# Kernel optimization log

Measured on AMD Instinct MI355X. Metric: run time of the kernel, lower is better.

## Reference

```python
import jax, jax.numpy as jnp
import numpy as np
from jax import nn as jnn

N = 100000      # nodes
E = 3200000     # edges (avg degree 32)
G = 1024        # graphs in batch
F_IN = 3        # num_features (hard-coded in module)
D = 32          # dim (hard-coded in module)
BN_EPS = 1e-5


def setup_inputs() -> dict:
    key = jax.random.key(0)
    ks = jax.random.split(key, 24)
    def lin(k, i, o):
        return (jax.random.normal(k, (i, o), jnp.float32) / np.sqrt(i)).astype(jnp.float32)
    inp = {}
    inp["x"] = jax.random.normal(ks[0], (N, F_IN), jnp.float32)
    inp["edge_index"] = jax.random.randint(ks[1], (2, E), 0, N, dtype=jnp.int32)
    inp["batch"] = jnp.sort(jax.random.randint(ks[2], (N,), 0, G, dtype=jnp.int32))
    idx = 3
    in_dims = [F_IN, D, D]
    for l in (1, 2, 3):
        inp[f"W{l}a"] = lin(ks[idx], in_dims[l - 1], D); idx += 1
        inp[f"b{l}a"] = jnp.zeros((D,), jnp.float32)
        inp[f"W{l}b"] = lin(ks[idx], D, D); idx += 1
        inp[f"b{l}b"] = jnp.zeros((D,), jnp.float32)
        inp[f"g{l}"] = jnp.ones((D,), jnp.float32)            # BN gamma
        inp[f"be{l}"] = jnp.zeros((D,), jnp.float32)          # BN beta
        inp[f"m{l}"] = 0.1 * jax.random.normal(ks[idx], (D,), jnp.float32); idx += 1  # running mean
        inp[f"v{l}"] = jax.random.uniform(ks[idx], (D,), jnp.float32, 0.5, 1.5); idx += 1  # running var
    inp["Wf1"] = lin(ks[idx], D, D); idx += 1
    inp["bf1"] = jnp.zeros((D,), jnp.float32)
    inp["Wf2"] = lin(ks[idx], D, 1)
    inp["bf2"] = jnp.zeros((1,), jnp.float32)
    return inp


def reference(x, edge_index, batch,
              W1a, b1a, W1b, b1b, g1, be1, m1, v1,
              W2a, b2a, W2b, b2b, g2, be2, m2, v2,
              W3a, b3a, W3b, b3b, g3, be3, m3, v3,
              Wf1, bf1, Wf2, bf2):
    src, dst = edge_index[0], edge_index[1]

    def gin_bn(h, Wa, ba, Wb, bb, g, be, m, v):
        # GINConv (eps=0): nn(x + sum_{j->i} x_j); then relu; then BatchNorm1d (eval stats)
        agg = jax.ops.segment_sum(h[src], dst, num_segments=N) + h  # [N, d]
        h2 = jnn.relu(agg @ Wa + ba) @ Wb + bb                      # 2-layer MLP
        h2 = jnn.relu(h2)
        return g * (h2 - m) * jax.lax.rsqrt(v + BN_EPS) + be

    h = gin_bn(x, W1a, b1a, W1b, b1b, g1, be1, m1, v1)
    h = gin_bn(h, W2a, b2a, W2b, b2b, g2, be2, m2, v2)
    h = gin_bn(h, W3a, b3a, W3b, b3b, g3, be3, m3, v3)
    p = jax.ops.segment_sum(h, batch, num_segments=G)   # global_add_pool -> [G, D]
    p = jnn.relu(p @ Wf1 + bf1)
    # dropout p=0.5 is identity at inference
    return jnp.tanh(p @ Wf2 + bf2)                      # [G, 1]
```

## Files before the change

### kernel.cpp

```cpp
#include <hip/hip_runtime.h>
#include <math.h>

#define D 32
#define BN_EPS 1e-5f
#define NRANGE 512
#define RWC 196
#define MAXD 80
#define EPB 8192
#define K1_TPB 512
#define EPT (EPB / K1_TPB)
#define PCH 8

__global__ __launch_bounds__(K1_TPB) void build_part(
    const int* __restrict__ src, const int* __restrict__ dst,
    unsigned int* __restrict__ part, int* __restrict__ gcount,
    int E, int cap, int RW, unsigned long long M) {
    __shared__ unsigned int sorted[EPB];
    __shared__ unsigned short rid[EPB];
    __shared__ int cnt[NRANGE];
    __shared__ int exc[NRANGE];
    __shared__ int cur[NRANGE];
    __shared__ int gbase[NRANGE];
    int t = threadIdx.x;
    cnt[t] = 0;
    __syncthreads();

    int base = blockIdx.x * EPB;
    int n = min(EPB, E - base);

    unsigned int mypk[EPT];
    unsigned short myr[EPT];
#pragma unroll
    for (int k = 0; k < EPT; k++) {
        int i = t + k * K1_TPB;
        if (i < n) {
            int d = dst[base + i];
            int s = src[base + i];
            int r = (int)(((unsigned long long)d * M) >> 40);
            mypk[k] = ((unsigned)(d - r * RW) << 17) | (unsigned)s;
            myr[k] = (unsigned short)r;
            atomicAdd(&cnt[r], 1);
        } else myr[k] = 0xFFFFu;
    }
    __syncthreads();

    int inc = cnt[t];
    exc[t] = inc;
    __syncthreads();
    for (int s = 1; s < NRANGE; s <<= 1) {
        int u = (t >= s) ? exc[t - s] : 0;
        __syncthreads();
        exc[t] += u;
        __syncthreads();
    }
    int excl = exc[t] - cnt[t];
    __syncthreads();
    exc[t] = excl;
    cur[t] = excl;
    gbase[t] = atomicAdd(&gcount[t], cnt[t]);
    __syncthreads();

#pragma unroll
    for (int k = 0; k < EPT; k++) {
        if (myr[k] != 0xFFFFu) {
            int j = atomicAdd(&cur[myr[k]], 1);
            sorted[j] = mypk[k];
            rid[j] = myr[k];
        }
    }
    __syncthreads();

    for (int j = t; j < n; j += K1_TPB) {
        int r = rid[j];
        int pos = gbase[r] + (j - exc[r]);
        if (pos < cap) part[(size_t)r * cap + pos] = sorted[j];
    }
}

__global__ __launch_bounds__(1024) void build_csr(
    const unsigned int* __restrict__ part, const int* __restrict__ gcount,
    int* __restrict__ col, int* __restrict__ deg,
    int cap, int RW, int N, int maxd) {
    __shared__ int bucket[RWC * MAXD];
    __shared__ int rank_[RWC];
    int r = blockIdx.x, t = threadIdx.x, T = blockDim.x;
    for (int i = t; i < RW; i += T) rank_[i] = 0;
    __syncthreads();

    int count = gcount[r]; if (count > cap) count = cap;
    const unsigned int* p = part + (size_t)r * cap;
    int nbase = r * RW;
    for (int i = t; i < count; i += T) {
        unsigned int v = p[i];
        int dl = (int)(v >> 17);
        int slot = atomicAdd(&rank_[dl], 1);
        if (slot < maxd) bucket[dl * maxd + slot] = (int)(v & 0x1FFFFu);
    }
    __syncthreads();

    for (int i = t; i < RW; i += T) {
        int rk = rank_[i]; if (rk > maxd) rk = maxd;
        int pdg = (rk + 15) & ~15; if (pdg > maxd) pdg = maxd;
        int self = nbase + i;
        for (int k = rk; k < pdg; k++) bucket[i * maxd + k] = self;
    }
    __syncthreads();

    int nvalid = N - nbase; if (nvalid > RW) nvalid = RW;
    if (nvalid <= 0) return;
    int words = nvalid * maxd;
    int4* dst4 = (int4*)&col[(size_t)nbase * maxd];
    const int4* src4 = (const int4*)bucket;
    int nq = words >> 2;
    for (int i = t; i < nq; i += T) dst4[i] = src4[i];
    for (int i = t; i < nvalid; i += T) {
        int rk = rank_[i];
        deg[nbase + i] = rk < maxd ? rk : maxd;
    }
}

__global__ void compute_y(const float* __restrict__ x, const float* __restrict__ W1a,
                          float* __restrict__ y, int N) {
    long long gid = (long long)blockIdx.x * blockDim.x + threadIdx.x;
    int i = (int)(gid >> 5);
    int lane = (int)(gid & 31);
    if (i >= N) return;
    float x0 = x[i * 3 + 0], x1 = x[i * 3 + 1], x2 = x[i * 3 + 2];
    float t = x0 * W1a[0 * D + lane];
    t = fmaf(x1, W1a[1 * D + lane], t);
    t = fmaf(x2, W1a[2 * D + lane], t);
    y[(size_t)i * D + lane] = t;
}

template <bool SKIP_WA>
__global__ void layer_fused(const float* __restrict__ hin, const int* __restrict__ deg,
                            const int* __restrict__ col, int maxd,
                            const float* __restrict__ Wa, const float* __restrict__ ba,
                            const float* __restrict__ Wb, const float* __restrict__ bb,
                            const float* __restrict__ g, const float* __restrict__ be,
                            const float* __restrict__ m, const float* __restrict__ v,
                            float* __restrict__ hout, int N) {
    long long gid = (long long)blockIdx.x * blockDim.x + threadIdx.x;
    int i = (int)(gid >> 5);
    int lane = (int)(gid & 31);
    if (i >= N) return;

    int dg = deg[i];
    if (dg > maxd) dg = maxd;
    int pdg = (dg + 15) & ~15; if (pdg > maxd) pdg = maxd;
    float acc = hin[(size_t)i * D + lane] * (float)(1 + dg - pdg);
    const int* cp = &col[(size_t)i * maxd];
    int e = 0;
    for (; e + 32 <= pdg; e += 32) {
        int4 c0 = *(const int4*)&cp[e];
        int4 c1 = *(const int4*)&cp[e + 4];
        int4 c2 = *(const int4*)&cp[e + 8];
        int4 c3 = *(const int4*)&cp[e + 12];
        int4 c4 = *(const int4*)&cp[e + 16];
        int4 c5 = *(const int4*)&cp[e + 20];
        int4 c6 = *(const int4*)&cp[e + 24];
        int4 c7 = *(const int4*)&cp[e + 28];
        float a0 = hin[(size_t)c0.x * D + lane];
        float a1 = hin[(size_t)c0.y * D + lane];
        float a2 = hin[(size_t)c0.z * D + lane];
        float a3 = hin[(size_t)c0.w * D + lane];
        float a4 = hin[(size_t)c1.x * D + lane];
        float a5 = hin[(size_t)c1.y * D + lane];
        float a6 = hin[(size_t)c1.z * D + lane];
        float a7 = hin[(size_t)c1.w * D + lane];
        float a8 = hin[(size_t)c2.x * D + lane];
        float a9 = hin[(size_t)c2.y * D + lane];
        float a10 = hin[(size_t)c2.z * D + lane];
        float a11 = hin[(size_t)c2.w * D + lane];
        float a12 = hin[(size_t)c3.x * D + lane];
        float a13 = hin[(size_t)c3.y * D + lane];
        float a14 = hin[(size_t)c3.z * D + lane];
        float a15 = hin[(size_t)c3.w * D + lane];
        float a16 = hin[(size_t)c4.x * D + lane];
        float a17 = hin[(size_t)c4.y * D + lane];
        float a18 = hin[(size_t)c4.z * D + lane];
        float a19 = hin[(size_t)c4.w * D + lane];
        float a20 = hin[(size_t)c5.x * D + lane];
        float a21 = hin[(size_t)c5.y * D + lane];
        float a22 = hin[(size_t)c5.z * D + lane];
        float a23 = hin[(size_t)c5.w * D + lane];
        float a24 = hin[(size_t)c6.x * D + lane];
        float a25 = hin[(size_t)c6.y * D + lane];
        float a26 = hin[(size_t)c6.z * D + lane];
        float a27 = hin[(size_t)c6.w * D + lane];
        float a28 = hin[(size_t)c7.x * D + lane];
        float a29 = hin[(size_t)c7.y * D + lane];
        float a30 = hin[(size_t)c7.z * D + lane];
        float a31 = hin[(size_t)c7.w * D + lane];
        acc += (((a0 + a1) + (a2 + a3)) + ((a4 + a5) + (a6 + a7))) +
               (((a8 + a9) + (a10 + a11)) + ((a12 + a13) + (a14 + a15))) +
               (((a16 + a17) + (a18 + a19)) + ((a20 + a21) + (a22 + a23))) +
               (((a24 + a25) + (a26 + a27)) + ((a28 + a29) + (a30 + a31)));
    }
    for (; e + 16 <= pdg; e += 16) {
        int4 c0 = *(const int4*)&cp[e];
        int4 c1 = *(const int4*)&cp[e + 4];
        int4 c2 = *(const int4*)&cp[e + 8];
        int4 c3 = *(const int4*)&cp[e + 12];
        float a0 = hin[(size_t)c0.x * D + lane];
        float a1 = hin[(size_t)c0.y * D + lane];
        float a2 = hin[(size_t)c0.z * D + lane];
        float a3 = hin[(size_t)c0.w * D + lane];
        float a4 = hin[(size_t)c1.x * D + lane];
        float a5 = hin[(size_t)c1.y * D + lane];
        float a6 = hin[(size_t)c1.z * D + lane];
        float a7 = hin[(size_t)c1.w * D + lane];
        float a8 = hin[(size_t)c2.x * D + lane];
        float a9 = hin[(size_t)c2.y * D + lane];
        float aa = hin[(size_t)c2.z * D + lane];
        float ab = hin[(size_t)c2.w * D + lane];
        float ac = hin[(size_t)c3.x * D + lane];
        float ad = hin[(size_t)c3.y * D + lane];
        float ae = hin[(size_t)c3.z * D + lane];
        float af = hin[(size_t)c3.w * D + lane];
        acc += ((a0 + a1) + (a2 + a3)) + ((a4 + a5) + (a6 + a7)) +
               (((a8 + a9) + (aa + ab)) + ((ac + ad) + (ae + af)));
    }

    float t;
    if (SKIP_WA) {
        t = fmaxf(acc + ba[lane], 0.f);
    } else {
        t = ba[lane];
#pragma unroll
        for (int k = 0; k < D; k++) {
            float ak = __shfl(acc, k, D);
            t = fmaf(ak, Wa[k * D + lane], t);
        }
        t = fmaxf(t, 0.f);
    }
    float o = bb[lane];
#pragma unroll
    for (int j = 0; j < D; j++) {
        float tj = __shfl(t, j, D);
        o = fmaf(tj, Wb[j * D + lane], o);
    }
    o = fmaxf(o, 0.f);
    hout[(size_t)i * D + lane] =
        g[lane] * (o - m[lane]) * rsqrtf(v[lane] + BN_EPS) + be[lane];
}

__device__ __forceinline__ int lower_bound_i(const int* a, int n, int key) {
    int lo = 0, hi = n;
    while (lo < hi) {
        int mid = (lo + hi) >> 1;
        if (a[mid] < key) lo = mid + 1; else hi = mid;
    }
    return lo;
}

__global__ void pool_partial(const float* __restrict__ h, const int* __restrict__ batch,
                             float* __restrict__ pool, int N, int G) {
    long long gid = (long long)blockIdx.x * blockDim.x + threadIdx.x;
    int grp = (int)(gid >> 5);
    int lane = (int)(gid & 31);
    int gi = grp / PCH;
    int c = grp - gi * PCH;
    if (gi >= G) return;
    int lo = lower_bound_i(batch, N, gi);
    int hi = lower_bound_i(batch, N, gi + 1);
    int len = hi - lo;
    if (len <= 0) return;
    int chunk = (len + PCH - 1) / PCH;
    int s = lo + c * chunk;
    int e = s + chunk; if (e > hi) e = hi;
    if (s >= e) return;
    float p = 0.f;
    for (int n = s; n < e; n++) p += h[(size_t)n * D + lane];
    atomicAdd(&pool[(size_t)gi * D + lane], p);
}

__global__ void head_kernel(const float* __restrict__ pool, const float* __restrict__ Wf1,
                            const float* __restrict__ bf1, const float* __restrict__ Wf2,
                            const float* __restrict__ bf2, float* __restrict__ out, int G) {
    long long gid = (long long)blockIdx.x * blockDim.x + threadIdx.x;
    int gi = (int)(gid >> 5);
    int lane = (int)(gid & 31);
    if (gi >= G) return;
    float p = pool[(size_t)gi * D + lane];
    float q = bf1[lane];
#pragma unroll
    for (int j = 0; j < D; j++) {
        float pj = __shfl(p, j, D);
        q = fmaf(pj, Wf1[j * D + lane], q);
    }
    q = fmaxf(q, 0.f);
    float r = q * Wf2[lane];
#pragma unroll
    for (int off = 16; off; off >>= 1) r += __shfl_xor(r, off, D);
    if (lane == 0) out[gi] = tanhf(r + bf2[0]);
}

extern "C" void kernel_launch(void* const* d_in, const int* in_sizes, int n_in,
                              void* d_out, int out_size, void* d_ws, size_t ws_size,
                              hipStream_t stream) {
    const float* x = (const float*)d_in[0];
    const int* ei = (const int*)d_in[1];
    const int* batch = (const int*)d_in[2];
    const int E = in_sizes[1] / 2;
    const int N = in_sizes[2];
    const int G = out_size;
    const int* src = ei;
    const int* dst = ei + E;

    const float* P[3][8];
    for (int l = 0; l < 3; l++)
        for (int k = 0; k < 8; k++) P[l][k] = (const float*)d_in[3 + 8 * l + k];
    const float* Wf1 = (const float*)d_in[27];
    const float* bf1 = (const float*)d_in[28];
    const float* Wf2 = (const float*)d_in[29];
    const float* bf2 = (const float*)d_in[30];

    const int RW = (N + NRANGE - 1) / NRANGE;
    const unsigned long long M = ((1ull << 40) + RW - 1) / RW;
    int mean = (E + NRANGE - 1) / NRANGE;
    int cap = mean + mean / 8 + 64;
    cap = (cap + 7) & ~7;

    float* ws = (float*)d_ws;
    size_t off = 0;
    float* h0 = ws + off; off += (size_t)N * D;
    float* h1 = ws + off; off += (size_t)N * D;
    unsigned int* part = (unsigned int*)h0;
    int* deg = (int*)(ws + off); off += N;
    int* gcount = (int*)(ws + off); off += NRANGE;
    float* pool = ws + off; off += (size_t)G * D;
    int* col = (int*)(ws + off);
    size_t remaining = ws_size / 4 > off ? ws_size / 4 - off : 0;
    int maxd = (int)(remaining / (size_t)N);
    if (maxd > MAXD) maxd = MAXD;
    maxd &= ~15;
    if (maxd < 16) maxd = 16;

    const int B = 256;
    long long tN32 = (long long)N * D;
    int nbp = (E + EPB - 1) / EPB;

    hipMemsetAsync(gcount, 0, NRANGE * sizeof(int), stream);
    build_part<<<nbp, K1_TPB, 0, stream>>>(src, dst, part, gcount, E, cap, RW, M);
    build_csr<<<NRANGE, 1024, 0, stream>>>(part, gcount, col, deg, cap, RW, N, maxd);

    compute_y<<<(int)((tN32 + B - 1) / B), B, 0, stream>>>(x, P[0][0], h0, N);
    layer_fused<true><<<(int)((tN32 + B - 1) / B), B, 0, stream>>>(
        h0, deg, col, maxd, P[0][0], P[0][1], P[0][2], P[0][3],
        P[0][4], P[0][5], P[0][6], P[0][7], h1, N);

    layer_fused<false><<<(int)((tN32 + B - 1) / B), B, 0, stream>>>(
        h1, deg, col, maxd, P[1][0], P[1][1], P[1][2], P[1][3],
        P[1][4], P[1][5], P[1][6], P[1][7], h0, N);

    layer_fused<false><<<(int)((tN32 + B - 1) / B), B, 0, stream>>>(
        h0, deg, col, maxd, P[2][0], P[2][1], P[2][2], P[2][3],
        P[2][4], P[2][5], P[2][6], P[2][7], h1, N);

    hipMemsetAsync(pool, 0, (size_t)G * D * sizeof(float), stream);
    pool_partial<<<(int)(((long long)G * PCH * 32 + B - 1) / B), B, 0, stream>>>(
        h1, batch, pool, N, G);
    head_kernel<<<(int)(((long long)G * D + B - 1) / B), B, 0, stream>>>(
        pool, Wf1, bf1, Wf2, bf2, (float*)d_out, G);
}
```

Baseline: 361.0 us.

## Fuse CSR build with first GIN layer, use wave-shuffle scan, merge memsets

```diff
diff --git a/kernel.cpp b/kernel.cpp
--- a/kernel.cpp
+++ b/kernel.cpp
@@ -21,6 +21,7 @@
     __shared__ int exc[NRANGE];
     __shared__ int cur[NRANGE];
     __shared__ int gbase[NRANGE];
+    __shared__ int wsum[K1_TPB / 64];
     int t = threadIdx.x;
     cnt[t] = 0;
     __syncthreads();
@@ -45,16 +46,21 @@
     __syncthreads();
 
     int inc = cnt[t];
-    exc[t] = inc;
-    __syncthreads();
-    for (int s = 1; s < NRANGE; s <<= 1) {
-        int u = (t >= s) ? exc[t - s] : 0;
-        __syncthreads();
-        exc[t] += u;
-        __syncthreads();
-    }
-    int excl = exc[t] - cnt[t];
-    __syncthreads();
+    int v = inc;
+#pragma unroll
+    for (int s = 1; s < 64; s <<= 1) {
+        int u = __shfl_up(v, s, 64);
+        if ((t & 63) >= s) v += u;
+    }
+    if ((t & 63) == 63) wsum[t >> 6] = v;
+    __syncthreads();
+    if (t == 0) {
+        int acc = 0;
+#pragma unroll
+        for (int w = 0; w < K1_TPB / 64; w++) { int tmp = wsum[w]; wsum[w] = acc; acc += tmp; }
+    }
+    __syncthreads();
+    int excl = v - inc + wsum[t >> 6];
     exc[t] = excl;
     cur[t] = excl;
     gbase[t] = atomicAdd(&gcount[t], cnt[t]);
@@ -74,48 +80,6 @@
         int r = rid[j];
         int pos = gbase[r] + (j - exc[r]);
         if (pos < cap) part[(size_t)r * cap + pos] = sorted[j];
-    }
-}
-
-__global__ __launch_bounds__(1024) void build_csr(
-    const unsigned int* __restrict__ part, const int* __restrict__ gcount,
-    int* __restrict__ col, int* __restrict__ deg,
-    int cap, int RW, int N, int maxd) {
-    __shared__ int bucket[RWC * MAXD];
-    __shared__ int rank_[RWC];
-    int r = blockIdx.x, t = threadIdx.x, T = blockDim.x;
-    for (int i = t; i < RW; i += T) rank_[i] = 0;
-    __syncthreads();
-
-    int count = gcount[r]; if (count > cap) count = cap;
-    const unsigned int* p = part + (size_t)r * cap;
-    int nbase = r * RW;
-    for (int i = t; i < count; i += T) {
-        unsigned int v = p[i];
-        int dl = (int)(v >> 17);
-        int slot = atomicAdd(&rank_[dl], 1);
-        if (slot < maxd) bucket[dl * maxd + slot] = (int)(v & 0x1FFFFu);
-    }
-    __syncthreads();
-
-    for (int i = t; i < RW; i += T) {
-        int rk = rank_[i]; if (rk > maxd) rk = maxd;
-        int pdg = (rk + 15) & ~15; if (pdg > maxd) pdg = maxd;
-        int self = nbase + i;
-        for (int k = rk; k < pdg; k++) bucket[i * maxd + k] = self;
-    }
-    __syncthreads();
-
-    int nvalid = N - nbase; if (nvalid > RW) nvalid = RW;
-    if (nvalid <= 0) return;
-    int words = nvalid * maxd;
-    int4* dst4 = (int4*)&col[(size_t)nbase * maxd];
-    const int4* src4 = (const int4*)bucket;
-    int nq = words >> 2;
-    for (int i = t; i < nq; i += T) dst4[i] = src4[i];
-    for (int i = t; i < nvalid; i += T) {
-        int rk = rank_[i];
-        deg[nbase + i] = rk < maxd ? rk : maxd;
     }
 }
 
@@ -132,7 +96,143 @@
     y[(size_t)i * D + lane] = t;
 }
 
-template <bool SKIP_WA>
+__global__ __launch_bounds__(1024) void layer1_csr(
+    const unsigned int* __restrict__ part, const int* __restrict__ gcount,
+    int* __restrict__ col, int* __restrict__ deg,
+    const float* __restrict__ y,
+    const float* __restrict__ ba, const float* __restrict__ Wb,
+    const float* __restrict__ bb, const float* __restrict__ g,
+    const float* __restrict__ be, const float* __restrict__ m,
+    const float* __restrict__ v, float* __restrict__ hout,
+    int cap, int RW, int N, int maxd) {
+    __shared__ int bucket[RWC * MAXD];
+    __shared__ int rank_[RWC];
+    int r = blockIdx.x, t = threadIdx.x, T = blockDim.x;
+    for (int i = t; i < RW; i += T) rank_[i] = 0;
+    __syncthreads();
+
+    int count = gcount[r]; if (count > cap) count = cap;
+    const unsigned int* p = part + (size_t)r * cap;
+    int nbase = r * RW;
+    for (int i = t; i < count; i += T) {
+        unsigned int pk = p[i];
+        int dl = (int)(pk >> 17);
+        int slot = atomicAdd(&rank_[dl], 1);
+        if (slot < maxd) bucket[dl * maxd + slot] = (int)(pk & 0x1FFFFu);
+    }
+    __syncthreads();
+
+    for (int i = t; i < RW; i += T) {
+        int rk = rank_[i]; if (rk > maxd) rk = maxd;
+        int pdg = (rk + 15) & ~15; if (pdg > maxd) pdg = maxd;
+        int self = nbase + i;
+        for (int k = rk; k < pdg; k++) bucket[i * maxd + k] = self;
+    }
+    __syncthreads();
+
+    int nvalid = N - nbase; if (nvalid > RW) nvalid = RW;
+    if (nvalid <= 0) return;
+    int words = nvalid * maxd;
+    int4* dst4 = (int4*)&col[(size_t)nbase * maxd];
+    const int4* src4 = (const int4*)bucket;
+    int nq = words >> 2;
+    for (int i = t; i < nq; i += T) dst4[i] = src4[i];
+    for (int i = t; i < nvalid; i += T) {
+        int rk = rank_[i];
+        deg[nbase + i] = rk < maxd ? rk : maxd;
+    }
+
+    int gidx = t >> 5, lane = t & 31;
+    for (int nl = gidx; nl < nvalid; nl += 32) {
+        int node = nbase + nl;
+        int dg = rank_[nl]; if (dg > maxd) dg = maxd;
+        int pdg = (dg + 15) & ~15; if (pdg > maxd) pdg = maxd;
+        float acc = y[(size_t)node * D + lane] * (float)(1 + dg - pdg);
+        const int* cp = &bucket[nl * maxd];
+        int e = 0;
+        for (; e + 32 <= pdg; e += 32) {
+            int4 c0 = *(const int4*)&cp[e];
+            int4 c1 = *(const int4*)&cp[e + 4];
+            int4 c2 = *(const int4*)&cp[e + 8];
+            int4 c3 = *(const int4*)&cp[e + 12];
+            int4 c4 = *(const int4*)&cp[e + 16];
+            int4 c5 = *(const int4*)&cp[e + 20];
+            int4 c6 = *(const int4*)&cp[e + 24];
+            int4 c7 = *(const int4*)&cp[e + 28];
+            float a0 = y[(size_t)c0.x * D + lane];
+            float a1 = y[(size_t)c0.y * D + lane];
+            float a2 = y[(size_t)c0.z * D + lane];
+            float a3 = y[(size_t)c0.w * D + lane];
+            float a4 = y[(size_t)c1.x * D + lane];
+            float a5 = y[(size_t)c1.y * D + lane];
+            float a6 = y[(size_t)c1.z * D + lane];
+            float a7 = y[(size_t)c1.w * D + lane];
+            float a8 = y[(size_t)c2.x * D + lane];
+            float a9 = y[(size_t)c2.y * D + lane];
+            float a10 = y[(size_t)c2.z * D + lane];
+            float a11 = y[(size_t)c2.w * D + lane];
+            float a12 = y[(size_t)c3.x * D + lane];
+            float a13 = y[(size_t)c3.y * D + lane];
+            float a14 = y[(size_t)c3.z * D + lane];
+            float a15 = y[(size_t)c3.w * D + lane];
+            float a16 = y[(size_t)c4.x * D + lane];
+            float a17 = y[(size_t)c4.y * D + lane];
+            float a18 = y[(size_t)c4.z * D + lane];
+            float a19 = y[(size_t)c4.w * D + lane];
+            float a20 = y[(size_t)c5.x * D + lane];
+            float a21 = y[(size_t)c5.y * D + lane];
+            float a22 = y[(size_t)c5.z * D + lane];
+            float a23 = y[(size_t)c5.w * D + lane];
+            float a24 = y[(size_t)c6.x * D + lane];
+            float a25 = y[(size_t)c6.y * D + lane];
+            float a26 = y[(size_t)c6.z * D + lane];
+            float a27 = y[(size_t)c6.w * D + lane];
+            float a28 = y[(size_t)c7.x * D + lane];
+            float a29 = y[(size_t)c7.y * D + lane];
+            float a30 = y[(size_t)c7.z * D + lane];
+            float a31 = y[(size_t)c7.w * D + lane];
+            acc += (((a0 + a1) + (a2 + a3)) + ((a4 + a5) + (a6 + a7))) +
+                   (((a8 + a9) + (a10 + a11)) + ((a12 + a13) + (a14 + a15))) +
+                   (((a16 + a17) + (a18 + a19)) + ((a20 + a21) + (a22 + a23))) +
+                   (((a24 + a25) + (a26 + a27)) + ((a28 + a29) + (a30 + a31)));
+        }
+        for (; e + 16 <= pdg; e += 16) {
+            int4 c0 = *(const int4*)&cp[e];
+            int4 c1 = *(const int4*)&cp[e + 4];
+            int4 c2 = *(const int4*)&cp[e + 8];
+            int4 c3 = *(const int4*)&cp[e + 12];
+            float a0 = y[(size_t)c0.x * D + lane];
+            float a1 = y[(size_t)c0.y * D + lane];
+            float a2 = y[(size_t)c0.z * D + lane];
+            float a3 = y[(size_t)c0.w * D + lane];
+            float a4 = y[(size_t)c1.x * D + lane];
+            float a5 = y[(size_t)c1.y * D + lane];
+            float a6 = y[(size_t)c1.z * D + lane];
+            float a7 = y[(size_t)c1.w * D + lane];
+            float a8 = y[(size_t)c2.x * D + lane];
+            float a9 = y[(size_t)c2.y * D + lane];
+            float aa = y[(size_t)c2.z * D + lane];
+            float ab = y[(size_t)c2.w * D + lane];
+            float ac = y[(size_t)c3.x * D + lane];
+            float ad = y[(size_t)c3.y * D + lane];
+            float ae = y[(size_t)c3.z * D + lane];
+            float af = y[(size_t)c3.w * D + lane];
+            acc += ((a0 + a1) + (a2 + a3)) + ((a4 + a5) + (a6 + a7)) +
+                   (((a8 + a9) + (aa + ab)) + ((ac + ad) + (ae + af)));
+        }
+        float tv = fmaxf(acc + ba[lane], 0.f);
+        float o = bb[lane];
+#pragma unroll
+        for (int j = 0; j < D; j++) {
+            float tj = __shfl(tv, j, D);
+            o = fmaf(tj, Wb[j * D + lane], o);
+        }
+        o = fmaxf(o, 0.f);
+        hout[(size_t)node * D + lane] =
+            g[lane] * (o - m[lane]) * rsqrtf(v[lane] + BN_EPS) + be[lane];
+    }
+}
+
 __global__ void layer_fused(const float* __restrict__ hin, const int* __restrict__ deg,
                             const int* __restrict__ col, int maxd,
                             const float* __restrict__ Wa, const float* __restrict__ ba,
@@ -222,18 +322,13 @@
                (((a8 + a9) + (aa + ab)) + ((ac + ad) + (ae + af)));
     }
 
-    float t;
-    if (SKIP_WA) {
-        t = fmaxf(acc + ba[lane], 0.f);
-    } else {
-        t = ba[lane];
-#pragma unroll
-        for (int k = 0; k < D; k++) {
-            float ak = __shfl(acc, k, D);
-            t = fmaf(ak, Wa[k * D + lane], t);
-        }
-        t = fmaxf(t, 0.f);
-    }
+    float t = ba[lane];
+#pragma unroll
+    for (int k = 0; k < D; k++) {
+        float ak = __shfl(acc, k, D);
+        t = fmaf(ak, Wa[k * D + lane], t);
+    }
+    t = fmaxf(t, 0.f);
     float o = bb[lane];
 #pragma unroll
     for (int j = 0; j < D; j++) {
@@ -326,7 +421,7 @@
     size_t off = 0;
     float* h0 = ws + off; off += (size_t)N * D;
     float* h1 = ws + off; off += (size_t)N * D;
-    unsigned int* part = (unsigned int*)h0;
+    unsigned int* part = (unsigned int*)(ws + off); off += (size_t)NRANGE * cap;
     int* deg = (int*)(ws + off); off += N;
     int* gcount = (int*)(ws + off); off += NRANGE;
     float* pool = ws + off; off += (size_t)G * D;
@@ -341,24 +436,21 @@
     long long tN32 = (long long)N * D;
     int nbp = (E + EPB - 1) / EPB;
 
-    hipMemsetAsync(gcount, 0, NRANGE * sizeof(int), stream);
+    hipMemsetAsync(gcount, 0, (NRANGE + (size_t)G * D) * sizeof(int), stream);
+    compute_y<<<(int)((tN32 + B - 1) / B), B, 0, stream>>>(x, P[0][0], h0, N);
     build_part<<<nbp, K1_TPB, 0, stream>>>(src, dst, part, gcount, E, cap, RW, M);
-    build_csr<<<NRANGE, 1024, 0, stream>>>(part, gcount, col, deg, cap, RW, N, maxd);
-
-    compute_y<<<(int)((tN32 + B - 1) / B), B, 0, stream>>>(x, P[0][0], h0, N);
-    layer_fused<true><<<(int)((tN32 + B - 1) / B), B, 0, stream>>>(
-        h0, deg, col, maxd, P[0][0], P[0][1], P[0][2], P[0][3],
-        P[0][4], P[0][5], P[0][6], P[0][7], h1, N);
-
-    layer_fused<false><<<(int)((tN32 + B - 1) / B), B, 0, stream>>>(
+    layer1_csr<<<NRANGE, 1024, 0, stream>>>(
+        part, gcount, col, deg, h0, P[0][1], P[0][2], P[0][3],
+        P[0][4], P[0][5], P[0][6], P[0][7], h1, cap, RW, N, maxd);
+
+    layer_fused<<<(int)((tN32 + B - 1) / B), B, 0, stream>>>(
         h1, deg, col, maxd, P[1][0], P[1][1], P[1][2], P[1][3],
         P[1][4], P[1][5], P[1][6], P[1][7], h0, N);
 
-    layer_fused<false><<<(int)((tN32 + B - 1) / B), B, 0, stream>>>(
+    layer_fused<<<(int)((tN32 + B - 1) / B), B, 0, stream>>>(
         h0, deg, col, maxd, P[2][0], P[2][1], P[2][2], P[2][3],
         P[2][4], P[2][5], P[2][6], P[2][7], h1, N);
 
-    hipMemsetAsync(pool, 0, (size_t)G * D * sizeof(float), stream);
     pool_partial<<<(int)(((long long)G * PCH * 32 + B - 1) / B), B, 0, stream>>>(
         h1, batch, pool, N, G);
     head_kernel<<<(int)(((long long)G * D + B - 1) / B), B, 0, stream>>>(
```

Result: faster. 353.1 us (-2.2%).
